# Optimization experiments

Measured on AMD Instinct MI355X. Metric: run time of the kernel, lower is better.

Reference implementation:

```python
import jax, jax.numpy as jnp
import numpy as np

B, H, W, C, NH = 400, 14, 14, 768, 12
HD = C // NH  # 64


def setup_inputs() -> dict:
    key = jax.random.key(0)
    ks = jax.random.split(key, 6)
    s = 0.02
    return {
        "hidden_states": jax.random.normal(ks[0], (B, H, W, C), jnp.float32),
        "qkv_w": jax.random.normal(ks[1], (3 * C, C), jnp.float32) * s,
        "qkv_b": jnp.zeros((3 * C,), jnp.float32),
        "proj_w": jax.random.normal(ks[2], (C, C), jnp.float32) * s,
        "proj_b": jnp.zeros((C,), jnp.float32),
        "rel_pos_h": jax.random.normal(ks[3], (2 * H - 1, HD), jnp.float32) * s,
        "rel_pos_w": jax.random.normal(ks[4], (2 * W - 1, HD), jnp.float32) * s,
    }


def _get_rel_pos(q_size, k_size, rel_pos):
    # q_size == k_size and table already has 2*k-1 entries -> pure gather,
    # matching SamVisionAttention.get_rel_pos without interpolation.
    coords = jnp.arange(q_size)[:, None] - jnp.arange(k_size)[None, :] + (k_size - 1)
    return rel_pos[coords]  # (q, k, head_dim)


def reference(hidden_states, qkv_w, qkv_b, proj_w, proj_b, rel_pos_h, rel_pos_w):
    b, h, w, c = hidden_states.shape
    scale = HD ** -0.5
    # qkv projection: (b, h*w, 3c) -> (3, b, nh, hw, hd)
    qkv = hidden_states.reshape(b, h * w, c) @ qkv_w.T + qkv_b
    qkv = qkv.reshape(b, h * w, 3, NH, HD).transpose(2, 0, 3, 1, 4)
    q, k, v = qkv[0], qkv[1], qkv[2]
    # decomposed relative position bias (computed from UNSCALED q, as in SAM)
    Rh = _get_rel_pos(h, h, rel_pos_h)  # (h, h, hd)
    Rw = _get_rel_pos(w, w, rel_pos_w)  # (w, w, hd)
    qr = q.reshape(b, NH, h, w, HD)
    rel_h = jnp.einsum('bnhwc,hkc->bnhwk', qr, Rh)  # (b, nh, h, w, h)
    rel_w = jnp.einsum('bnhwc,wkc->bnhwk', qr, Rw)  # (b, nh, h, w, w)
    bias = (rel_h[..., :, None] + rel_w[..., None, :]).reshape(b, NH, h * w, h * w)
    # attention
    attn = jnp.einsum('bnqd,bnkd->bnqk', q, k) * scale + bias
    attn = jax.nn.softmax(attn, axis=-1)
    out = jnp.einsum('bnqk,bnkd->bnqd', attn, v)
    out = out.transpose(0, 2, 1, 3).reshape(b, h, w, c)
    return out @ proj_w.T + proj_b
```

## Files before the change

kernel.cpp:

```cpp
#include <hip/hip_runtime.h>
#include <hip/hip_bf16.h>

typedef __bf16 bfv8 __attribute__((ext_vector_type(8)));
typedef __bf16 bfv4 __attribute__((ext_vector_type(4)));
typedef float f32x4 __attribute__((ext_vector_type(4)));
typedef unsigned int u32x2 __attribute__((ext_vector_type(2)));
typedef unsigned short u16;
typedef unsigned int u32;

#define MT 78400

#define SBAR() __builtin_amdgcn_s_barrier()
#define VMCNT(n) asm volatile("s_waitcnt vmcnt(" #n ")" ::: "memory")

__device__ __forceinline__ u16 f2bf(float f) {
  u32 x = __float_as_uint(f);
  return (u16)((x + 0x7FFFu + ((x >> 16) & 1u)) >> 16);
}

__device__ __forceinline__ void gld16(const void* g, void* l) {
  __builtin_amdgcn_global_load_lds((const __attribute__((address_space(1))) void*)g,
                                   (__attribute__((address_space(3))) void*)l, 16, 0, 0);
}

__global__ __launch_bounds__(256) void cvt_f32_bf16(const float* __restrict__ src,
                                                    u16* __restrict__ dst, int n8) {
  int stride = gridDim.x * 256;
  for (int i = blockIdx.x * 256 + threadIdx.x; i < n8; i += stride) {
    const float4* s = (const float4*)(src + (long)i * 8);
    float4 a = s[0], b = s[1];
    u32 p0 = f2bf(a.x) | ((u32)f2bf(a.y) << 16);
    u32 p1 = f2bf(a.z) | ((u32)f2bf(a.w) << 16);
    u32 p2 = f2bf(b.x) | ((u32)f2bf(b.y) << 16);
    u32 p3 = f2bf(b.z) | ((u32)f2bf(b.w) << 16);
    uint4 o = {p0, p1, p2, p3};
    *(uint4*)(dst + (long)i * 8) = o;
  }
}

__global__ __launch_bounds__(256) void indk_init(u16* __restrict__ T) {
  int i = blockIdx.x * 256 + threadIdx.x;
  if (i < 208 * 40) {
    int k = i / 40, j = i - (i / 40) * 40;
    int hk = k / 14, wk = k - hk * 14;
    T[i] = (j == hk || j == 16 + wk) ? 0x3F80 : 0;
  }
}

__device__ __forceinline__ void gemm256_main(const u16* __restrict__ A, const u16* __restrict__ W,
                                             u16* SH, int m0, int n0, int tid,
                                             f32x4 (&acc)[8][4]) {
  const int lane = tid & 63;
  const int q15 = lane & 15, g = lane >> 4;
  const int wid = tid >> 6;
  const int wm = wid >> 2, wn = wid & 3;
  const int x0 = (g ^ (q15 & 7)) << 3;
  const int arow0 = wm * 128 + q15;
  const int brow0 = wn * 64 + q15;

  const int r0 = tid >> 3;
  const int gc0 = ((tid & 7) ^ (r0 & 7)) << 3;
  int ra00 = m0 + r0;       if (ra00 > MT - 1) ra00 = MT - 1;
  int ra10 = m0 + 64 + r0;  if (ra10 > MT - 1) ra10 = MT - 1;
  int ra01 = m0 + 128 + r0; if (ra01 > MT - 1) ra01 = MT - 1;
  int ra11 = m0 + 192 + r0; if (ra11 > MT - 1) ra11 = MT - 1;
  const u16* aS00 = A + (long)ra00 * 768 + gc0;
  const u16* aS10 = A + (long)ra10 * 768 + gc0;
  const u16* aS01 = A + (long)ra01 * 768 + gc0;
  const u16* aS11 = A + (long)ra11 * 768 + gc0;
  const u16* bS00 = W + (long)(n0 + r0) * 768 + gc0;
  const u16* bS10 = W + (long)(n0 + 64 + r0) * 768 + gc0;
  const u16* bS01 = W + (long)(n0 + 128 + r0) * 768 + gc0;
  const u16* bS11 = W + (long)(n0 + 192 + r0) * 768 + gc0;
  u16* dA = SH + tid * 8;
  u16* dB = dA + 16384;

  auto STGA = [&](int sl, const u16* p0, const u16* p1, int hoff, int kt) {
    u16* d = dA + sl * 32768 + hoff;
    gld16(p0 + kt * 64, d);
    gld16(p1 + kt * 64, d + 4096);
  };
  auto STGB = [&](int sl, const u16* p0, const u16* p1, int hoff, int kt) {
    u16* d = dB + sl * 32768 + hoff;
    gld16(p0 + kt * 64, d);
    gld16(p1 + kt * 64, d + 4096);
  };

  bfv8 b0[4], b1[4];
  bfv8 aX0[2], aX1[2], aY0[2], aY1[2];

  STGB(0, bS00, bS10, 0, 0); STGB(0, bS01, bS11, 8192, 0);
  STGA(0, aS00, aS10, 0, 0); STGA(0, aS01, aS11, 8192, 0);
  STGB(1, bS00, bS10, 0, 1); STGB(1, bS01, bS11, 8192, 1);
  STGA(1, aS00, aS10, 0, 1);
  VMCNT(4);
  SBAR();
  {
    const u16* Sb = SH + 16384;
#pragma unroll
    for (int ni = 0; ni < 4; ++ni) {
      const u16* bp = Sb + (brow0 + ni * 16) * 64;
      b0[ni] = *(const bfv8*)(bp + x0);
      b1[ni] = *(const bfv8*)(bp + (x0 ^ 32));
    }
#pragma unroll
    for (int m2 = 0; m2 < 2; ++m2) {
      const u16* ap = SH + (arow0 + m2 * 16) * 64;
      aX0[m2] = *(const bfv8*)(ap + x0);
      aX1[m2] = *(const bfv8*)(ap + (x0 ^ 32));
    }
  }

  for (int u = 0; u < 12; ++u) {
    const int sl = u & 1;
    const u16* Sa = SH + sl * 32768;
    const u16* San = SH + (sl ^ 1) * 32768;
    const u16* Sbn = San + 16384;
    const int kn1 = (u + 1 < 12) ? u + 1 : 11;
    const int kn2 = (u + 2 < 12) ? u + 2 : 11;

    __builtin_amdgcn_s_setprio(1);
#pragma unroll
    for (int m2 = 0; m2 < 2; ++m2)
#pragma unroll
      for (int ni = 0; ni < 4; ++ni)
        acc[m2][ni] = __builtin_amdgcn_mfma_f32_16x16x32_bf16(aX0[m2], b0[ni], acc[m2][ni], 0, 0, 0);
#pragma unroll
    for (int m2 = 0; m2 < 2; ++m2)
#pragma unroll
      for (int ni = 0; ni < 4; ++ni)
        acc[m2][ni] = __builtin_amdgcn_mfma_f32_16x16x32_bf16(aX1[m2], b1[ni], acc[m2][ni], 0, 0, 0);
    __builtin_amdgcn_s_setprio(0);
    SBAR();
#pragma unroll
    for (int m2 = 0; m2 < 2; ++m2) {
      const u16* ap = Sa + (arow0 + (2 + m2) * 16) * 64;
      aY0[m2] = *(const bfv8*)(ap + x0);
      aY1[m2] = *(const bfv8*)(ap + (x0 ^ 32));
    }
    STGA(sl ^ 1, aS01, aS11, 8192, kn1);

    __builtin_amdgcn_s_setprio(1);
#pragma unroll
    for (int m2 = 0; m2 < 2; ++m2)
#pragma unroll
      for (int ni = 0; ni < 4; ++ni)
        acc[2 + m2][ni] = __builtin_amdgcn_mfma_f32_16x16x32_bf16(aY0[m2], b0[ni], acc[2 + m2][ni], 0, 0, 0);
#pragma unroll
    for (int m2 = 0; m2 < 2; ++m2)
#pragma unroll
      for (int ni = 0; ni < 4; ++ni)
        acc[2 + m2][ni] = __builtin_amdgcn_mfma_f32_16x16x32_bf16(aY1[m2], b1[ni], acc[2 + m2][ni], 0, 0, 0);
    __builtin_amdgcn_s_setprio(0);
    SBAR();
#pragma unroll
    for (int m2 = 0; m2 < 2; ++m2) {
      const u16* ap = Sa + (arow0 + (4 + m2) * 16) * 64;
      aX0[m2] = *(const bfv8*)(ap + x0);
      aX1[m2] = *(const bfv8*)(ap + (x0 ^ 32));
    }
    STGB(sl, bS00, bS10, 0, kn2);

    __builtin_amdgcn_s_setprio(1);
#pragma unroll
    for (int m2 = 0; m2 < 2; ++m2)
#pragma unroll
      for (int ni = 0; ni < 4; ++ni)
        acc[4 + m2][ni] = __builtin_amdgcn_mfma_f32_16x16x32_bf16(aX0[m2], b0[ni], acc[4 + m2][ni], 0, 0, 0);
#pragma unroll
    for (int m2 = 0; m2 < 2; ++m2)
#pragma unroll
      for (int ni = 0; ni < 4; ++ni)
        acc[4 + m2][ni] = __builtin_amdgcn_mfma_f32_16x16x32_bf16(aX1[m2], b1[ni], acc[4 + m2][ni], 0, 0, 0);
    __builtin_amdgcn_s_setprio(0);
    SBAR();
#pragma unroll
    for (int m2 = 0; m2 < 2; ++m2) {
      const u16* ap = Sa + (arow0 + (6 + m2) * 16) * 64;
      aY0[m2] = *(const bfv8*)(ap + x0);
      aY1[m2] = *(const bfv8*)(ap + (x0 ^ 32));
    }
    STGB(sl, bS01, bS11, 8192, kn2);

    __builtin_amdgcn_s_setprio(1);
#pragma unroll
    for (int m2 = 0; m2 < 2; ++m2)
#pragma unroll
      for (int ni = 0; ni < 4; ++ni)
        acc[6 + m2][ni] = __builtin_amdgcn_mfma_f32_16x16x32_bf16(aY0[m2], b0[ni], acc[6 + m2][ni], 0, 0, 0);
#pragma unroll
    for (int m2 = 0; m2 < 2; ++m2)
#pragma unroll
      for (int ni = 0; ni < 4; ++ni)
        acc[6 + m2][ni] = __builtin_amdgcn_mfma_f32_16x16x32_bf16(aY1[m2], b1[ni], acc[6 + m2][ni], 0, 0, 0);
    __builtin_amdgcn_s_setprio(0);
    VMCNT(4);
    SBAR();
    if (u < 11) {
#pragma unroll
      for (int ni = 0; ni < 4; ++ni) {
        const u16* bp = Sbn + (brow0 + ni * 16) * 64;
        b0[ni] = *(const bfv8*)(bp + x0);
        b1[ni] = *(const bfv8*)(bp + (x0 ^ 32));
      }
#pragma unroll
      for (int m2 = 0; m2 < 2; ++m2) {
        const u16* ap = San + (arow0 + m2 * 16) * 64;
        aX0[m2] = *(const bfv8*)(ap + x0);
        aX1[m2] = *(const bfv8*)(ap + (x0 ^ 32));
      }
    }
    STGA(sl, aS00, aS10, 0, kn2);
  }
  VMCNT(0);
}

__global__ __launch_bounds__(512, 2) void qkv_gemm(const u16* __restrict__ A, const u16* __restrict__ W,
                                                   const float* __restrict__ bias,
                                                   u16* __restrict__ Qo, u16* __restrict__ Ko,
                                                   u16* __restrict__ Vo) {
  extern __shared__ u16 SH[];
  const int tid = threadIdx.x;
  const int orig = blockIdx.x;
  const int xcd = orig & 7, ii = orig >> 3;
  const int wg = (xcd < 3 ? xcd * 346 : 1038 + (xcd - 3) * 345) + ii;
  const int mt = wg / 9, nt = wg - mt * 9;
  const int m0 = mt * 256, n0 = nt * 256;

  f32x4 acc[8][4];
#pragma unroll
  for (int i = 0; i < 8; ++i)
#pragma unroll
    for (int j = 0; j < 4; ++j) acc[i][j] = (f32x4){0.f, 0.f, 0.f, 0.f};

  gemm256_main(A, W, SH, m0, n0, tid, acc);

  const int lane = tid & 63, q15 = lane & 15, g = lane >> 4;
  const int wid = tid >> 6, wm = wid >> 2, wn = wid & 3;
  __syncthreads();
  const int sel = nt / 3;
  u16* dst = (sel == 0) ? Qo : (sel == 1) ? Ko : Vo;
  const int ntr = nt - sel * 3;
  u16* Cs = SH;

#pragma unroll
  for (int h = 0; h < 2; ++h) {
    if (wm == h) {
#pragma unroll
      for (int ni = 0; ni < 4; ++ni) {
        int col = wn * 64 + ni * 16 + q15;
        float bb = bias[n0 + col];
#pragma unroll
        for (int mi = 0; mi < 8; ++mi)
#pragma unroll
          for (int r = 0; r < 4; ++r)
            Cs[(mi * 16 + g * 4 + r) * 264 + col] = f2bf(acc[mi][ni][r] + bb);
      }
    }
    __syncthreads();
#pragma unroll
    for (int j = 0; j < 8; ++j) {
      int idx = tid + 512 * j;
      int row = idx >> 5, cc = idx & 31;
      int m = m0 + h * 128 + row;
      if (m < MT) {
        int b = m / 196, s = m - b * 196;
        int nh = ntr * 4 + (cc >> 3);
        int hd0 = (cc & 7) * 8;
        uint4 v = *(const uint4*)(Cs + row * 264 + cc * 8);
        *(uint4*)(dst + (long)b * 150528 + (long)s * 64 + nh * 12544 + hd0) = v;
      }
    }
    if (h == 0) __syncthreads();
  }
}

__global__ __launch_bounds__(512, 2) void proj_gemm(const u16* __restrict__ A, const u16* __restrict__ W,
                                                    const float* __restrict__ bias,
                                                    float* __restrict__ out) {
  extern __shared__ u16 SH[];
  const int tid = threadIdx.x;
  const int orig = blockIdx.x;
  const int xcd = orig & 7, ii = orig >> 3;
  const int wg = (xcd < 1 ? xcd * 116 : 116 + (xcd - 1) * 115) + ii;
  const int mt = wg / 3, nt = wg - mt * 3;
  const int m0 = mt * 256, n0 = nt * 256;

  f32x4 acc[8][4];
#pragma unroll
  for (int i = 0; i < 8; ++i)
#pragma unroll
    for (int j = 0; j < 4; ++j) acc[i][j] = (f32x4){0.f, 0.f, 0.f, 0.f};

  gemm256_main(A, W, SH, m0, n0, tid, acc);

  const int lane = tid & 63, q15 = lane & 15, g = lane >> 4;
  const int wid = tid >> 6, wm = wid >> 2, wn = wid & 3;

#pragma unroll
  for (int ni = 0; ni < 4; ++ni) {
    int n = n0 + wn * 64 + ni * 16 + q15;
    float bb = bias[n];
#pragma unroll
    for (int mi = 0; mi < 8; ++mi)
#pragma unroll
      for (int r = 0; r < 4; ++r) {
        int m = m0 + wm * 128 + mi * 16 + g * 4 + r;
        if (m < MT) out[(long)m * 768 + n] = acc[mi][ni][r] + bb;
      }
  }
}

#define KLDS_OFF 0
#define VT_OFF   26624
#define TH_OFF   59392
#define TW_OFF   63280
#define AW_OFF   67168
#define SMEM_SZ  77408

__global__ __launch_bounds__(512, 2) void attn_kernel(const u16* __restrict__ Q, const u16* __restrict__ K,
                                                      const u16* __restrict__ V,
                                                      const float* __restrict__ rph, const float* __restrict__ rpw,
                                                      const u16* __restrict__ IndKg,
                                                      u16* __restrict__ AO) {
  extern __shared__ char smem[];
  u16* Klds = (u16*)(smem + KLDS_OFF);
  u16* VT = (u16*)(smem + VT_OFF);
  u16* TH = (u16*)(smem + TH_OFF);
  u16* TW = (u16*)(smem + TW_OFF);
  const int tid = threadIdx.x, lane = tid & 63, wid = tid >> 6;
  const int q15 = lane & 15, g = lane >> 4;
  const int bnh = blockIdx.x;
  const int b = bnh / 12, nh = bnh - b * 12;
  const u16* Qg = Q + bnh * 12544;
  const u16* Kg = K + bnh * 12544;
  const u16* Vg = V + bnh * 12544;
  u16* AWw = (u16*)(smem + AW_OFF) + wid * 16 * 40;

  for (int c = tid; c < 1568; c += 512) {
    int krow = c >> 3, part = c & 7;
    gld16(Kg + krow * 64 + ((part ^ (krow & 7)) << 3), Klds + c * 8);
  }
  for (int idx = tid; idx < 1792; idx += 512) {
    int k = idx >> 3, nb = idx & 7;
    u32 w0 = 0, w1 = 0, w2 = 0, w3 = 0;
    if (k < 196) {
      uint4 t = *(const uint4*)(Vg + k * 64 + nb * 8);
      w0 = t.x; w1 = t.y; w2 = t.z; w3 = t.w;
    }
    u32 wv[4] = {w0, w1, w2, w3};
#pragma unroll
    for (int j = 0; j < 8; j++) {
      int n = nb * 8 + j;
      u16 val = (u16)(wv[j >> 1] >> ((j & 1) * 16));
      int blk = (k >> 3) ^ (n & 7) ^ (n >> 3);
      VT[n * 256 + blk * 8 + (k & 7)] = val;
    }
  }
  for (int i = tid; i < 27 * 64; i += 512) {
    int r = i >> 6, cc = i & 63;
    TH[r * 72 + cc] = f2bf(rph[i]);
    TW[r * 72 + cc] = f2bf(rpw[i]);
  }
  __syncthreads();

  const int ksw = q15 & 7;
  const int ko0 = (g ^ ksw) << 3;
  const int ko1 = ((g + 4) ^ ksw) << 3;
  const f32x4 zero = {0.f, 0.f, 0.f, 0.f};

  auto mk_qaug = [&](int tq0, bfv8 qf0, bfv8 qf1) -> bfv8 {
    int hq0 = tq0 / 14, hq1 = (tq0 + 15) / 14;
    int rha = hq0 + 13 - q15; rha = rha < 0 ? 0 : (rha > 26 ? 26 : rha);
    int rhb = hq1 + 13 - q15; rhb = rhb < 0 ? 0 : (rhb > 26 ? 26 : rhb);
    int rwa = q15;
    int rwb = 16 + q15; if (rwb > 26) rwb = 26;
    f32x4 c0h = zero, c1h = zero, c0w = zero, c1w = zero;
    {
      bfv8 t0 = *(const bfv8*)(TH + rha * 72 + g * 8);
      bfv8 t1 = *(const bfv8*)(TH + rha * 72 + 32 + g * 8);
      c0h = __builtin_amdgcn_mfma_f32_16x16x32_bf16(qf0, t0, c0h, 0, 0, 0);
      c0h = __builtin_amdgcn_mfma_f32_16x16x32_bf16(qf1, t1, c0h, 0, 0, 0);
      bfv8 t2 = *(const bfv8*)(TH + rhb * 72 + g * 8);
      bfv8 t3 = *(const bfv8*)(TH + rhb * 72 + 32 + g * 8);
      c1h = __builtin_amdgcn_mfma_f32_16x16x32_bf16(qf0, t2, c1h, 0, 0, 0);
      c1h = __builtin_amdgcn_mfma_f32_16x16x32_bf16(qf1, t3, c1h, 0, 0, 0);
      bfv8 u0 = *(const bfv8*)(TW + rwa * 72 + g * 8);
      bfv8 u1 = *(const bfv8*)(TW + rwa * 72 + 32 + g * 8);
      c0w = __builtin_amdgcn_mfma_f32_16x16x32_bf16(qf0, u0, c0w, 0, 0, 0);
      c0w = __builtin_amdgcn_mfma_f32_16x16x32_bf16(qf1, u1, c0w, 0, 0, 0);
      bfv8 u2 = *(const bfv8*)(TW + rwb * 72 + g * 8);
      bfv8 u3 = *(const bfv8*)(TW + rwb * 72 + 32 + g * 8);
      c1w = __builtin_amdgcn_mfma_f32_16x16x32_bf16(qf0, u2, c1w, 0, 0, 0);
      c1w = __builtin_amdgcn_mfma_f32_16x16x32_bf16(qf1, u3, c1w, 0, 0, 0);
    }
#pragma unroll
    for (int r = 0; r < 4; r++) {
      int row = g * 4 + r;
      int qq = tq0 + row;
      int hqr = qq / 14;
      int wq_r = qq - hqr * 14;
      if (q15 < 10) AWw[row * 40 + 30 + q15] = 0;
      float rh = ((hqr == hq1) ? c1h[r] : c0h[r]) * 8.0f;
      AWw[row * 40 + q15] = (q15 <= 13) ? f2bf(rh) : (u16)0;
      int w0p = wq_r + 13 - q15;
      if (w0p >= 0 && w0p <= 13) AWw[row * 40 + 16 + w0p] = f2bf(c0w[r] * 8.0f);
      int w1p = wq_r - 3 - q15;
      if (w1p >= 0 && w1p <= 13) AWw[row * 40 + 16 + w1p] = f2bf(c1w[r] * 8.0f);
    }
    return *(const bfv8*)(AWw + q15 * 40 + g * 8);
  };

  if (wid < 7) {
    const int q0 = wid * 32;
    int qrA = q0 + q15;      if (qrA > 195) qrA = 195;
    int qrB = q0 + 16 + q15; if (qrB > 195) qrB = 195;
    bfv8 qf0A = *(const bfv8*)(Qg + qrA * 64 + g * 8);
    bfv8 qf1A = *(const bfv8*)(Qg + qrA * 64 + 32 + g * 8);
    bfv8 qf0B = *(const bfv8*)(Qg + qrB * 64 + g * 8);
    bfv8 qf1B = *(const bfv8*)(Qg + qrB * 64 + 32 + g * 8);

    bfv8 qaugA = mk_qaug(q0, qf0A, qf1A);
    bfv8 qaugB = mk_qaug(q0 + 16, qf0B, qf1B);

    f32x4 oA[4] = {zero, zero, zero, zero};
    f32x4 oB[4] = {zero, zero, zero, zero};
    float denA = 0.f, denB = 0.f;
#pragma unroll
    for (int t = 0; t < 13; t++) {
      const u16* kr = Klds + (t * 16 + q15) * 64;
      bfv8 kb0 = *(const bfv8*)(kr + ko0);
      bfv8 kb1 = *(const bfv8*)(kr + ko1);
      bfv8 ib = *(const bfv8*)(IndKg + (t * 16 + q15) * 40 + g * 8);
      __builtin_amdgcn_s_setprio(1);
      f32x4 aA = __builtin_amdgcn_mfma_f32_16x16x32_bf16(ib, qaugA, zero, 0, 0, 0);
      f32x4 aB = __builtin_amdgcn_mfma_f32_16x16x32_bf16(ib, qaugB, zero, 0, 0, 0);
      aA = __builtin_amdgcn_mfma_f32_16x16x32_bf16(kb0, qf0A, aA, 0, 0, 0);
      aB = __builtin_amdgcn_mfma_f32_16x16x32_bf16(kb0, qf0B, aB, 0, 0, 0);
      f32x4 sA = __builtin_amdgcn_mfma_f32_16x16x32_bf16(kb1, qf1A, aA, 0, 0, 0);
      f32x4 sB = __builtin_amdgcn_mfma_f32_16x16x32_bf16(kb1, qf1B, aB, 0, 0, 0);
      __builtin_amdgcn_s_setprio(0);
      const bool msk = (t == 12 && g > 0);
      float pA0 = msk ? 0.f : exp2f(sA[0] * 0.18033688f - 5.7707802f);
      float pA1 = msk ? 0.f : exp2f(sA[1] * 0.18033688f - 5.7707802f);
      float pA2 = msk ? 0.f : exp2f(sA[2] * 0.18033688f - 5.7707802f);
      float pA3 = msk ? 0.f : exp2f(sA[3] * 0.18033688f - 5.7707802f);
      float pB0 = msk ? 0.f : exp2f(sB[0] * 0.18033688f - 5.7707802f);
      float pB1 = msk ? 0.f : exp2f(sB[1] * 0.18033688f - 5.7707802f);
      float pB2 = msk ? 0.f : exp2f(sB[2] * 0.18033688f - 5.7707802f);
      float pB3 = msk ? 0.f : exp2f(sB[3] * 0.18033688f - 5.7707802f);
      denA += (pA0 + pA1) + (pA2 + pA3);
      denB += (pB0 + pB1) + (pB2 + pB3);
      u32 loA, hiA, loB, hiB;
      asm("v_cvt_pk_bf16_f32 %0, %1, %2" : "=v"(loA) : "v"(pA0), "v"(pA1));
      asm("v_cvt_pk_bf16_f32 %0, %1, %2" : "=v"(hiA) : "v"(pA2), "v"(pA3));
      asm("v_cvt_pk_bf16_f32 %0, %1, %2" : "=v"(loB) : "v"(pB0), "v"(pB1));
      asm("v_cvt_pk_bf16_f32 %0, %1, %2" : "=v"(hiB) : "v"(pB2), "v"(pB3));
      u32x2 wA; wA.x = loA; wA.y = hiA;
      u32x2 wB; wB.x = loB; wB.y = hiB;
      bfv4 paA = __builtin_bit_cast(bfv4, wA);
      bfv4 paB = __builtin_bit_cast(bfv4, wB);
      const int kblk = 2 * t + (g >> 1);
      const int koff = (g & 1) * 4;
      __builtin_amdgcn_s_setprio(1);
#pragma unroll
      for (int nt_ = 0; nt_ < 4; nt_++) {
        int n = nt_ * 16 + q15;
        int blk = (kblk ^ (n & 7) ^ (n >> 3));
        bfv4 vb = *(const bfv4*)(VT + n * 256 + blk * 8 + koff);
        asm("v_mfma_f32_16x16x16_bf16 %0, %1, %2, %0" : "+v"(oA[nt_]) : "v"(paA), "v"(vb));
        asm("v_mfma_f32_16x16x16_bf16 %0, %1, %2, %0" : "+v"(oB[nt_]) : "v"(paB), "v"(vb));
      }
      __builtin_amdgcn_s_setprio(0);
    }
    denA += __shfl_xor(denA, 16);
    denA += __shfl_xor(denA, 32);
    denB += __shfl_xor(denB, 16);
    denB += __shfl_xor(denB, 32);
    float invA = 1.0f / denA, invB = 1.0f / denB;
    float invrA[4], invrB[4];
#pragma unroll
    for (int r = 0; r < 4; r++) {
      invrA[r] = __shfl(invA, g * 4 + r);
      invrB[r] = __shfl(invB, g * 4 + r);
    }

#pragma unroll
    for (int nt_ = 0; nt_ < 4; nt_++)
#pragma unroll
      for (int r = 0; r < 4; r++) {
        int sA_ = q0 + g * 4 + r;
        if (sA_ < 196)
          AO[((long)(b * 196 + sA_)) * 768 + nh * 64 + nt_ * 16 + q15] = f2bf(oA[nt_][r] * invrA[r]);
        int sB_ = q0 + 16 + g * 4 + r;
        if (sB_ < 196)
          AO[((long)(b * 196 + sB_)) * 768 + nh * 64 + nt_ * 16 + q15] = f2bf(oB[nt_][r] * invrB[r]);
      }
  }
}

#define GEMM_LDS 131072

extern "C" void kernel_launch(void* const* d_in, const int* in_sizes, int n_in,
                              void* d_out, int out_size, void* d_ws, size_t ws_size,
                              hipStream_t stream) {
  const float* hs = (const float*)d_in[0];
  const float* qkvw = (const float*)d_in[1];
  const float* qkvb = (const float*)d_in[2];
  const float* projw = (const float*)d_in[3];
  const float* projb = (const float*)d_in[4];
  const float* rph = (const float*)d_in[5];
  const float* rpw = (const float*)d_in[6];

  char* ws = (char*)d_ws;
  u16* Xb = (u16*)ws;
  u16* Wq = (u16*)(ws + 120422400);
  u16* Wp = (u16*)(ws + 123961344);
  u16* Qb = (u16*)(ws + 125140992);
  u16* Kb = (u16*)(ws + 245563392);
  u16* Vb = (u16*)(ws + 365985792);
  u16* AO = Xb;
  u16* IndKg = Wq;

  cvt_f32_bf16<<<2048, 256, 0, stream>>>(hs, Xb, 7526400);
  cvt_f32_bf16<<<864, 256, 0, stream>>>(qkvw, Wq, 221184);
  cvt_f32_bf16<<<288, 256, 0, stream>>>(projw, Wp, 73728);

  hipFuncSetAttribute((const void*)qkv_gemm, hipFuncAttributeMaxDynamicSharedMemorySize, GEMM_LDS);
  qkv_gemm<<<2763, 512, GEMM_LDS, stream>>>(Xb, Wq, qkvb, Qb, Kb, Vb);

  indk_init<<<33, 256, 0, stream>>>(IndKg);

  hipFuncSetAttribute((const void*)attn_kernel, hipFuncAttributeMaxDynamicSharedMemorySize, SMEM_SZ);
  attn_kernel<<<4800, 512, SMEM_SZ, stream>>>(Qb, Kb, Vb, rph, rpw, IndKg, AO);

  hipFuncSetAttribute((const void*)proj_gemm, hipFuncAttributeMaxDynamicSharedMemorySize, GEMM_LDS);
  proj_gemm<<<921, 512, GEMM_LDS, stream>>>(AO, Wp, projb, (float*)d_out);
}
```

Before: 744.6 us.

## Fuse fp32-to-bf16 conversion of hidden states into QKV GEMM A-tile loading

Drops the separate conversion kernel for the 240MB fp32 activation tensor. The QKV GEMM now loads fp32 A tiles into registers, converts them with packed bf16 instructions and writes them into LDS, instead of using direct global-to-LDS bf16 loads. This removes a full read and write pass over the activations. In exchange the GEMM loses async LDS loads for A, needs more registers (its launch bound drops the min-2-blocks hint), reads twice the bytes per A tile, and adds explicit waits and scheduling barriers.

```diff
diff --git a/kernel.cpp b/kernel.cpp
--- a/kernel.cpp
+++ b/kernel.cpp
@@ -12,6 +12,8 @@
 
 #define SBAR() __builtin_amdgcn_s_barrier()
 #define VMCNT(n) asm volatile("s_waitcnt vmcnt(" #n ")" ::: "memory")
+#define LGKM0() asm volatile("s_waitcnt lgkmcnt(0)" ::: "memory")
+#define SCHEDB() __builtin_amdgcn_sched_barrier(0)
 
 __device__ __forceinline__ u16 f2bf(float f) {
   u32 x = __float_as_uint(f);
@@ -21,6 +23,16 @@
 __device__ __forceinline__ void gld16(const void* g, void* l) {
   __builtin_amdgcn_global_load_lds((const __attribute__((address_space(1))) void*)g,
                                    (__attribute__((address_space(3))) void*)l, 16, 0, 0);
+}
+
+__device__ __forceinline__ void cvtwr(u16* d, f32x4 a, f32x4 b) {
+  u32 p0, p1, p2, p3;
+  asm("v_cvt_pk_bf16_f32 %0, %1, %2" : "=v"(p0) : "v"(a[0]), "v"(a[1]));
+  asm("v_cvt_pk_bf16_f32 %0, %1, %2" : "=v"(p1) : "v"(a[2]), "v"(a[3]));
+  asm("v_cvt_pk_bf16_f32 %0, %1, %2" : "=v"(p2) : "v"(b[0]), "v"(b[1]));
+  asm("v_cvt_pk_bf16_f32 %0, %1, %2" : "=v"(p3) : "v"(b[2]), "v"(b[3]));
+  uint4 o = {p0, p1, p2, p3};
+  *(uint4*)d = o;
 }
 
 __global__ __launch_bounds__(256) void cvt_f32_bf16(const float* __restrict__ src,
@@ -47,7 +59,8 @@
   }
 }
 
-__device__ __forceinline__ void gemm256_main(const u16* __restrict__ A, const u16* __restrict__ W,
+template<bool F32A>
+__device__ __forceinline__ void gemm256_core(const void* Ain, const u16* __restrict__ W,
                                              u16* SH, int m0, int n0, int tid,
                                              f32x4 (&acc)[8][4]) {
   const int lane = tid & 63;
@@ -59,41 +72,92 @@
   const int brow0 = wn * 64 + q15;
 
   const int r0 = tid >> 3;
-  const int gc0 = ((tid & 7) ^ (r0 & 7)) << 3;
-  int ra00 = m0 + r0;       if (ra00 > MT - 1) ra00 = MT - 1;
-  int ra10 = m0 + 64 + r0;  if (ra10 > MT - 1) ra10 = MT - 1;
-  int ra01 = m0 + 128 + r0; if (ra01 > MT - 1) ra01 = MT - 1;
-  int ra11 = m0 + 192 + r0; if (ra11 > MT - 1) ra11 = MT - 1;
-  const u16* aS00 = A + (long)ra00 * 768 + gc0;
-  const u16* aS10 = A + (long)ra10 * 768 + gc0;
-  const u16* aS01 = A + (long)ra01 * 768 + gc0;
-  const u16* aS11 = A + (long)ra11 * 768 + gc0;
+  const int cc8 = tid & 7;
+  const int gc0 = (cc8 ^ (r0 & 7)) << 3;
+  int ra0 = m0 + r0;       if (ra0 > MT - 1) ra0 = MT - 1;
+  int ra1 = m0 + 64 + r0;  if (ra1 > MT - 1) ra1 = MT - 1;
+  int ra2 = m0 + 128 + r0; if (ra2 > MT - 1) ra2 = MT - 1;
+  int ra3 = m0 + 192 + r0; if (ra3 > MT - 1) ra3 = MT - 1;
+
   const u16* bS00 = W + (long)(n0 + r0) * 768 + gc0;
   const u16* bS10 = W + (long)(n0 + 64 + r0) * 768 + gc0;
   const u16* bS01 = W + (long)(n0 + 128 + r0) * 768 + gc0;
   const u16* bS11 = W + (long)(n0 + 192 + r0) * 768 + gc0;
+  u16* dB = SH + 16384 + tid * 8;
+
+  auto STGB = [&](int sl, const u16* p0, const u16* p1, int hoff, int kt) {
+    u16* d = dB + sl * 32768 + hoff;
+    gld16(p0 + kt * 64, d);
+    gld16(p1 + kt * 64, d + 4096);
+  };
+
+  const u16* aS00 = nullptr; const u16* aS10 = nullptr;
+  const u16* aS01 = nullptr; const u16* aS11 = nullptr;
   u16* dA = SH + tid * 8;
-  u16* dB = dA + 16384;
-
+  const float* aF0 = nullptr; const float* aF1 = nullptr;
+  const float* aF2 = nullptr; const float* aF3 = nullptr;
+  u16* wd0 = SH + r0 * 64 + gc0;
+  if constexpr (F32A) {
+    const float* Af = (const float*)Ain;
+    aF0 = Af + (long)ra0 * 768 + cc8 * 8;
+    aF1 = Af + (long)ra1 * 768 + cc8 * 8;
+    aF2 = Af + (long)ra2 * 768 + cc8 * 8;
+    aF3 = Af + (long)ra3 * 768 + cc8 * 8;
+  } else {
+    const u16* Ab = (const u16*)Ain;
+    aS00 = Ab + (long)ra0 * 768 + gc0;
+    aS10 = Ab + (long)ra1 * 768 + gc0;
+    aS01 = Ab + (long)ra2 * 768 + gc0;
+    aS11 = Ab + (long)ra3 * 768 + gc0;
+  }
   auto STGA = [&](int sl, const u16* p0, const u16* p1, int hoff, int kt) {
     u16* d = dA + sl * 32768 + hoff;
     gld16(p0 + kt * 64, d);
     gld16(p1 + kt * 64, d + 4096);
   };
-  auto STGB = [&](int sl, const u16* p0, const u16* p1, int hoff, int kt) {
-    u16* d = dB + sl * 32768 + hoff;
-    gld16(p0 + kt * 64, d);
-    gld16(p1 + kt * 64, d + 4096);
+
+  f32x4 av0, av1, av2, av3, av4, av5, av6, av7;
+  auto LDA0 = [&](int kt) {
+    av0 = *(const f32x4*)(aF0 + kt * 64);
+    av1 = *(const f32x4*)(aF0 + kt * 64 + 4);
+    av2 = *(const f32x4*)(aF1 + kt * 64);
+    av3 = *(const f32x4*)(aF1 + kt * 64 + 4);
+  };
+  auto LDA1 = [&](int kt) {
+    av4 = *(const f32x4*)(aF2 + kt * 64);
+    av5 = *(const f32x4*)(aF2 + kt * 64 + 4);
+    av6 = *(const f32x4*)(aF3 + kt * 64);
+    av7 = *(const f32x4*)(aF3 + kt * 64 + 4);
+  };
+  auto WRA = [&](int sl) {
+    u16* d = wd0 + sl * 32768;
+    cvtwr(d, av0, av1);
+    cvtwr(d + 4096, av2, av3);
+    cvtwr(d + 8192, av4, av5);
+    cvtwr(d + 12288, av6, av7);
   };
 
   bfv8 b0[4], b1[4];
   bfv8 aX0[2], aX1[2], aY0[2], aY1[2];
 
-  STGB(0, bS00, bS10, 0, 0); STGB(0, bS01, bS11, 8192, 0);
-  STGA(0, aS00, aS10, 0, 0); STGA(0, aS01, aS11, 8192, 0);
-  STGB(1, bS00, bS10, 0, 1); STGB(1, bS01, bS11, 8192, 1);
-  STGA(1, aS00, aS10, 0, 1);
-  VMCNT(4);
+  if constexpr (F32A) {
+    LDA0(0); LDA1(0);
+    SCHEDB();
+    STGB(0, bS00, bS10, 0, 0); STGB(0, bS01, bS11, 8192, 0);
+    STGB(1, bS00, bS10, 0, 1); STGB(1, bS01, bS11, 8192, 1);
+    VMCNT(8);
+    WRA(0);
+    LDA0(1); LDA1(1);
+    VMCNT(0);
+    WRA(1);
+    LGKM0();
+  } else {
+    STGB(0, bS00, bS10, 0, 0); STGB(0, bS01, bS11, 8192, 0);
+    STGA(0, aS00, aS10, 0, 0); STGA(0, aS01, aS11, 8192, 0);
+    STGB(1, bS00, bS10, 0, 1); STGB(1, bS01, bS11, 8192, 1);
+    STGA(1, aS00, aS10, 0, 1);
+    VMCNT(4);
+  }
   SBAR();
   {
     const u16* Sb = SH + 16384;
@@ -138,7 +202,8 @@
       aY0[m2] = *(const bfv8*)(ap + x0);
       aY1[m2] = *(const bfv8*)(ap + (x0 ^ 32));
     }
-    STGA(sl ^ 1, aS01, aS11, 8192, kn1);
+    if constexpr (F32A) { LDA0(kn2); SCHEDB(); }
+    else STGA(sl ^ 1, aS01, aS11, 8192, kn1);
 
     __builtin_amdgcn_s_setprio(1);
 #pragma unroll
@@ -159,6 +224,7 @@
       aX0[m2] = *(const bfv8*)(ap + x0);
       aX1[m2] = *(const bfv8*)(ap + (x0 ^ 32));
     }
+    if constexpr (F32A) { LDA1(kn2); SCHEDB(); }
     STGB(sl, bS00, bS10, 0, kn2);
 
     __builtin_amdgcn_s_setprio(1);
@@ -196,6 +262,8 @@
     __builtin_amdgcn_s_setprio(0);
     VMCNT(4);
     SBAR();
+    if constexpr (F32A) { WRA(sl); LGKM0(); }
+    else STGA(sl, aS00, aS10, 0, kn2);
     if (u < 11) {
 #pragma unroll
       for (int ni = 0; ni < 4; ++ni) {
@@ -210,15 +278,14 @@
         aX1[m2] = *(const bfv8*)(ap + (x0 ^ 32));
       }
     }
-    STGA(sl, aS00, aS10, 0, kn2);
   }
   VMCNT(0);
 }
 
-__global__ __launch_bounds__(512, 2) void qkv_gemm(const u16* __restrict__ A, const u16* __restrict__ W,
-                                                   const float* __restrict__ bias,
-                                                   u16* __restrict__ Qo, u16* __restrict__ Ko,
-                                                   u16* __restrict__ Vo) {
+__global__ __launch_bounds__(512) void qkv_gemm(const float* __restrict__ A, const u16* __restrict__ W,
+                                                const float* __restrict__ bias,
+                                                u16* __restrict__ Qo, u16* __restrict__ Ko,
+                                                u16* __restrict__ Vo) {
   extern __shared__ u16 SH[];
   const int tid = threadIdx.x;
   const int orig = blockIdx.x;
@@ -233,7 +300,7 @@
 #pragma unroll
     for (int j = 0; j < 4; ++j) acc[i][j] = (f32x4){0.f, 0.f, 0.f, 0.f};
 
-  gemm256_main(A, W, SH, m0, n0, tid, acc);
+  gemm256_core<true>(A, W, SH, m0, n0, tid, acc);
 
   const int lane = tid & 63, q15 = lane & 15, g = lane >> 4;
   const int wid = tid >> 6, wm = wid >> 2, wn = wid & 3;
@@ -292,7 +359,7 @@
 #pragma unroll
     for (int j = 0; j < 4; ++j) acc[i][j] = (f32x4){0.f, 0.f, 0.f, 0.f};
 
-  gemm256_main(A, W, SH, m0, n0, tid, acc);
+  gemm256_core<false>(A, W, SH, m0, n0, tid, acc);
 
   const int lane = tid & 63, q15 = lane & 15, g = lane >> 4;
   const int wid = tid >> 6, wm = wid >> 2, wn = wid & 3;
@@ -522,12 +589,11 @@
   u16* AO = Xb;
   u16* IndKg = Wq;
 
-  cvt_f32_bf16<<<2048, 256, 0, stream>>>(hs, Xb, 7526400);
   cvt_f32_bf16<<<864, 256, 0, stream>>>(qkvw, Wq, 221184);
   cvt_f32_bf16<<<288, 256, 0, stream>>>(projw, Wp, 73728);
 
   hipFuncSetAttribute((const void*)qkv_gemm, hipFuncAttributeMaxDynamicSharedMemorySize, GEMM_LDS);
-  qkv_gemm<<<2763, 512, GEMM_LDS, stream>>>(Xb, Wq, qkvb, Qb, Kb, Vb);
+  qkv_gemm<<<2763, 512, GEMM_LDS, stream>>>(hs, Wq, qkvb, Qb, Kb, Vb);
 
   indk_init<<<33, 256, 0, stream>>>(IndKg);
 
```

Result: slower. 824.8 us (+10.8%).
